# Optimization experiments

Measured on AMD Instinct MI355X. Metric: run time of the kernel, lower is better.

The kernel has to match this reference:

```python
import jax, jax.numpy as jnp
import numpy as np
from jax import lax


def setup_inputs() -> dict:
    key = jax.random.key(0)
    k1, k2, k3 = jax.random.split(key, 3)
    B, T, D, H = 128, 1024, 512, 512
    x = jax.random.normal(k1, (B, T, D), dtype=jnp.float32)
    # scaled init to keep tanh out of hard saturation
    W_ih = jax.random.normal(k2, (D, H), dtype=jnp.float32) / np.sqrt(D)
    W_hh = jax.random.normal(k3, (H, H), dtype=jnp.float32) / np.sqrt(H)
    b = jnp.zeros((H,), dtype=jnp.float32)
    return {"x": x, "W_ih": W_ih, "W_hh": W_hh, "b": b}


def reference(x, W_ih, W_hh, b):
    # Vanilla RNN: h_t = tanh(x_t @ W_ih + h_{t-1} @ W_hh + b)
    # return_sequences=False -> final hidden state (batch, hidden)
    B = x.shape[0]
    H = W_hh.shape[0]
    # Precompute the large input-to-hidden projection for all timesteps at once.
    xp = jnp.einsum('btd,dh->bth', x, W_ih) + b  # (B, T, H)
    xp_t = jnp.swapaxes(xp, 0, 1)                # (T, B, H) for scan over time

    def step(h, xp_step):
        h_new = jnp.tanh(xp_step + h @ W_hh)
        return h_new, None

    h0 = jnp.zeros((B, H), dtype=x.dtype)
    h_final, _ = lax.scan(step, h0, xp_t)
    return h_final
```

## Files before the change

### kernel.cpp

```cpp
#include <hip/hip_runtime.h>
#include <hip/hip_fp16.h>

typedef _Float16 half8 __attribute__((ext_vector_type(8)));
typedef _Float16 half4v __attribute__((ext_vector_type(4)));
typedef float floatx4 __attribute__((ext_vector_type(4)));

constexpr int BN = 128;
constexpr int T  = 1024;
constexpr int D  = 512;
constexpr int H  = 512;

constexpr size_t OFF_WIHT  = 0;
constexpr size_t OFF_WHHT  = 524288;
constexpr size_t OFF_HX    = 1048576;
constexpr size_t OFF_FLAGS = 1048576 + 262144;
constexpr size_t OFF_XP    = 2097152;

__device__ __forceinline__ float fast_tanh(float x) {
    float e = __expf(2.0f * x);
    return 1.0f - 2.0f / (e + 1.0f);
}

struct u64x2_s { unsigned long long a, b; };

__global__ __launch_bounds__(256) void prep_transpose(
    const float* __restrict__ Wih, const float* __restrict__ Whh,
    _Float16* __restrict__ WihT, _Float16* __restrict__ WhhT,
    int* __restrict__ flags)
{
    if (blockIdx.x == 0 && blockIdx.y == 0 && blockIdx.z == 0 && threadIdx.x < 16)
        flags[threadIdx.x * 16] = -1;

    __shared__ float tile[32][33];
    const float* src = (blockIdx.z == 0) ? Wih : Whh;
    _Float16* dst    = (blockIdx.z == 0) ? WihT : WhhT;
    const int tx = threadIdx.x & 31;
    const int ty = threadIdx.x >> 5;
    const int kbase = blockIdx.y * 32;
    const int nbase = blockIdx.x * 32;
    for (int r = 0; r < 4; ++r)
        tile[ty + r * 8][tx] = src[(size_t)(kbase + ty + r * 8) * 512 + nbase + tx];
    __syncthreads();
    for (int r = 0; r < 4; ++r)
        dst[(size_t)(nbase + ty + r * 8) * 512 + kbase + tx] =
            (_Float16)tile[tx][ty + r * 8];
}

__global__ __launch_bounds__(256) void xp_gemm(
    const float* __restrict__ x, const _Float16* __restrict__ WT,
    const float* __restrict__ bias, _Float16* __restrict__ xp)
{
    __shared__ _Float16 As[128][40];
    __shared__ _Float16 Bs[128][40];
    const int tid  = threadIdx.x;
    const int lane = tid & 63;
    const int w    = tid >> 6;
    const int wm   = w & 1, wn = w >> 1;
    const int l15  = lane & 15, q = lane >> 4;
    const size_t mbase = (size_t)blockIdx.y * 128;
    const int    nbase = blockIdx.x * 128;

    floatx4 acc[4][4];
    for (int i = 0; i < 4; ++i)
        for (int j = 0; j < 4; ++j)
            acc[i][j] = (floatx4){0.f, 0.f, 0.f, 0.f};

    for (int kt = 0; kt < 16; ++kt) {
        const int k0 = kt * 32;
        {
            const int k4 = (tid & 7) * 4;
            const int row0 = tid >> 3;
            for (int r = 0; r < 4; ++r) {
                const int row = row0 + r * 32;
                const float4 v = *(const float4*)&x[(mbase + row) * D + k0 + k4];
                half4v hv;
                hv[0] = (_Float16)v.x; hv[1] = (_Float16)v.y;
                hv[2] = (_Float16)v.z; hv[3] = (_Float16)v.w;
                *(half4v*)&As[row][k4] = hv;
            }
        }
        {
            const int k8 = (tid & 3) * 8;
            const int n0 = tid >> 2;
            for (int r = 0; r < 2; ++r) {
                const int n = n0 + r * 64;
                *(half8*)&Bs[n][k8] =
                    *(const half8*)&WT[(size_t)(nbase + n) * D + k0 + k8];
            }
        }
        __syncthreads();
        half8 a[4], b[4];
        for (int i = 0; i < 4; ++i)
            a[i] = *(const half8*)&As[wm * 64 + i * 16 + l15][q * 8];
        for (int j = 0; j < 4; ++j)
            b[j] = *(const half8*)&Bs[wn * 64 + j * 16 + l15][q * 8];
        for (int i = 0; i < 4; ++i)
            for (int j = 0; j < 4; ++j)
                acc[i][j] = __builtin_amdgcn_mfma_f32_16x16x32_f16(
                    a[i], b[j], acc[i][j], 0, 0, 0);
        __syncthreads();
    }
    float bc[4];
    for (int j = 0; j < 4; ++j)
        bc[j] = bias[nbase + wn * 64 + j * 16 + l15];
    for (int i = 0; i < 4; ++i)
        for (int r = 0; r < 4; ++r) {
            const size_t row = mbase + wm * 64 + i * 16 + q * 4 + r;
            const int b_row = (int)(row >> 10);
            const int tt    = (int)(row & 1023);
            _Float16* dst = &xp[((size_t)tt * BN + b_row) * H];
            for (int j = 0; j < 4; ++j) {
                const int col = nbase + wn * 64 + j * 16 + l15;
                dst[col] = (_Float16)(acc[i][j][r] + bc[j]);
            }
        }
}

__global__ __launch_bounds__(512, 2) void rnn_scan(
    const _Float16* __restrict__ xp, const _Float16* __restrict__ WT,
    float* __restrict__ out, _Float16* __restrict__ hx, int* __restrict__ flags)
{
    __shared__ _Float16 hbuf[2][4096];

    const int bid  = blockIdx.x;
    const int half = bid >> 3;
    const int g    = bid & 7;
    const int peer16 = (bid ^ 8) * 16;
    const int bid16  = bid * 16;
    const int tid  = threadIdx.x;
    const int lane = tid & 63;
    const int w    = tid >> 6;
    const int l15  = lane & 15;
    const int q    = lane >> 4;

    const int nbase = half * 256 + w * 32;
    const _Float16* wr0 = WT + (size_t)(nbase + 0  + l15) * H + q * 8;
    const _Float16* wr1 = WT + (size_t)(nbase + 16 + l15) * H + q * 8;

    half8 wa[16][2];
#pragma unroll
    for (int j = 0; j < 16; ++j) {
        const int c = (j < 8) ? (half * 8 + j) : ((half ^ 1) * 8 + (j - 8));
        wa[j][0] = *(const half8*)&wr0[c * 32];
        wa[j][1] = *(const half8*)&wr1[c * 32];
        asm volatile("" : "+a"(wa[j][0]), "+a"(wa[j][1]));
    }

    const int ebase = ((w * 4 + (q >> 1)) * 16 + l15) * 8 + (q & 1) * 4;

    {
        const _Float16* x0 = xp + ((size_t)g * 16 + l15) * H + nbase + q * 4;
        half4v v0 = *(const half4v*)&x0[0];
        half4v v1 = *(const half4v*)&x0[16];
        half4v hn0, hn1;
#pragma unroll
        for (int r = 0; r < 4; ++r) {
            hn0[r] = (_Float16)fast_tanh((float)v0[r]);
            hn1[r] = (_Float16)fast_tanh((float)v1[r]);
        }
        _Float16* hxo = hx + ((size_t)(1 * 8 + g) * 2 + half) * 4096;
        __hip_atomic_store((unsigned long long*)hxo + (ebase >> 2),
                           __builtin_bit_cast(unsigned long long, hn0),
                           __ATOMIC_RELAXED, __HIP_MEMORY_SCOPE_AGENT);
        __hip_atomic_store((unsigned long long*)hxo + ((ebase + 256) >> 2),
                           __builtin_bit_cast(unsigned long long, hn1),
                           __ATOMIC_RELAXED, __HIP_MEMORY_SCOPE_AGENT);
        *(half4v*)&hbuf[1][ebase]       = hn0;
        *(half4v*)&hbuf[1][ebase + 256] = hn1;
        __syncthreads();
        if (tid == 0)
            __hip_atomic_store(&flags[bid16], 0, __ATOMIC_RELAXED,
                               __HIP_MEMORY_SCOPE_AGENT);
    }

    const _Float16* xlane = xp + ((size_t)g * 16 + l15) * H + nbase + q * 4;
    const int poff64 = q * 32 + l15 * 2;

    for (int t = 1; t < T; ++t) {
        int f = __hip_atomic_load(&flags[peer16], __ATOMIC_RELAXED,
                                  __HIP_MEMORY_SCOPE_AGENT);
        __builtin_amdgcn_sched_barrier(0);

        const _Float16* xt = xlane + (size_t)t * (BN * H);
        const half4v xpv0 = *(const half4v*)&xt[0];
        const half4v xpv1 = *(const half4v*)&xt[16];

        const _Float16* hbo = &hbuf[t & 1][(q * 16 + l15) * 8];
        half8 hfA[8];
#pragma unroll
        for (int c8 = 0; c8 < 8; ++c8)
            hfA[c8] = *(const half8*)&hbo[c8 * 512];
        floatx4 acc0 = (floatx4){0.f,0.f,0.f,0.f};
        floatx4 acc1 = (floatx4){0.f,0.f,0.f,0.f};
#pragma unroll
        for (int c8 = 0; c8 < 8; ++c8) {
            acc0 = __builtin_amdgcn_mfma_f32_16x16x32_f16(wa[c8][0], hfA[c8], acc0, 0, 0, 0);
            acc1 = __builtin_amdgcn_mfma_f32_16x16x32_f16(wa[c8][1], hfA[c8], acc1, 0, 0, 0);
        }

        if (f < t - 1) {
            do {
                __builtin_amdgcn_s_sleep(1);
                f = __hip_atomic_load(&flags[peer16], __ATOMIC_RELAXED,
                                      __HIP_MEMORY_SCOPE_AGENT);
            } while (f < t - 1);
        }
        asm volatile("" : "+v"(f));

        const unsigned long long* ps64 = (const unsigned long long*)hx
            + ((size_t)((t & 1) * 8 + g) * 2 + (half ^ 1)) * 1024
            + poff64 + (f >> 31);
        half8 hfB[8];
#pragma unroll
        for (int c8 = 0; c8 < 8; ++c8) {
            unsigned long long d0 = __hip_atomic_load(&ps64[c8 * 128 + 0],
                                    __ATOMIC_RELAXED, __HIP_MEMORY_SCOPE_AGENT);
            unsigned long long d1 = __hip_atomic_load(&ps64[c8 * 128 + 1],
                                    __ATOMIC_RELAXED, __HIP_MEMORY_SCOPE_AGENT);
            hfB[c8] = __builtin_bit_cast(half8, u64x2_s{d0, d1});
        }

#pragma unroll
        for (int c8 = 0; c8 < 8; ++c8) {
            acc0 = __builtin_amdgcn_mfma_f32_16x16x32_f16(wa[8 + c8][0], hfB[c8], acc0, 0, 0, 0);
            acc1 = __builtin_amdgcn_mfma_f32_16x16x32_f16(wa[8 + c8][1], hfB[c8], acc1, 0, 0, 0);
        }

        if (t < T - 1) {
            half4v hn0, hn1;
#pragma unroll
            for (int r = 0; r < 4; ++r) {
                hn0[r] = (_Float16)fast_tanh(acc0[r] + (float)xpv0[r]);
                hn1[r] = (_Float16)fast_tanh(acc1[r] + (float)xpv1[r]);
            }
            _Float16* hxo = hx + ((size_t)(((t + 1) & 1) * 8 + g) * 2 + half) * 4096;
            __hip_atomic_store((unsigned long long*)hxo + (ebase >> 2),
                               __builtin_bit_cast(unsigned long long, hn0),
                               __ATOMIC_RELAXED, __HIP_MEMORY_SCOPE_AGENT);
            __hip_atomic_store((unsigned long long*)hxo + ((ebase + 256) >> 2),
                               __builtin_bit_cast(unsigned long long, hn1),
                               __ATOMIC_RELAXED, __HIP_MEMORY_SCOPE_AGENT);
            _Float16* ho = hbuf[(t + 1) & 1];
            *(half4v*)&ho[ebase]       = hn0;
            *(half4v*)&ho[ebase + 256] = hn1;
            __syncthreads();
            if (tid == 0)
                __hip_atomic_store(&flags[bid16], t, __ATOMIC_RELAXED,
                                   __HIP_MEMORY_SCOPE_AGENT);
        } else {
            float4 o0, o1;
            o0.x = fast_tanh(acc0[0] + (float)xpv0[0]);
            o0.y = fast_tanh(acc0[1] + (float)xpv0[1]);
            o0.z = fast_tanh(acc0[2] + (float)xpv0[2]);
            o0.w = fast_tanh(acc0[3] + (float)xpv0[3]);
            o1.x = fast_tanh(acc1[0] + (float)xpv1[0]);
            o1.y = fast_tanh(acc1[1] + (float)xpv1[1]);
            o1.z = fast_tanh(acc1[2] + (float)xpv1[2]);
            o1.w = fast_tanh(acc1[3] + (float)xpv1[3]);
            float* ob = &out[((size_t)g * 16 + l15) * H + nbase + q * 4];
            *(float4*)&ob[0]  = o0;
            *(float4*)&ob[16] = o1;
        }
    }
}

extern "C" void kernel_launch(void* const* d_in, const int* in_sizes, int n_in,
                              void* d_out, int out_size, void* d_ws, size_t ws_size,
                              hipStream_t stream)
{
    const float* x   = (const float*)d_in[0];
    const float* Wih = (const float*)d_in[1];
    const float* Whh = (const float*)d_in[2];
    const float* b   = (const float*)d_in[3];
    float* out = (float*)d_out;

    char* ws = (char*)d_ws;
    _Float16* WihT = (_Float16*)(ws + OFF_WIHT);
    _Float16* WhhT = (_Float16*)(ws + OFF_WHHT);
    _Float16* hx   = (_Float16*)(ws + OFF_HX);
    int*      flags = (int*)(ws + OFF_FLAGS);
    _Float16* xp   = (_Float16*)(ws + OFF_XP);

    prep_transpose<<<dim3(16, 16, 2), 256, 0, stream>>>(Wih, Whh, WihT, WhhT, flags);
    xp_gemm<<<dim3(4, 1024), 256, 0, stream>>>(x, WihT, b, xp);
    rnn_scan<<<16, 512, 0, stream>>>(xp, WhhT, out, hx, flags);
}
```

Before: 3.574 ms.

## Replace flag-based peer handshake with tagged data words polled directly

```diff
diff --git a/kernel.cpp b/kernel.cpp
--- a/kernel.cpp
+++ b/kernel.cpp
@@ -4,32 +4,40 @@
 typedef _Float16 half8 __attribute__((ext_vector_type(8)));
 typedef _Float16 half4v __attribute__((ext_vector_type(4)));
 typedef float floatx4 __attribute__((ext_vector_type(4)));
+typedef unsigned int uint;
+typedef unsigned long long u64;
 
 constexpr int BN = 128;
 constexpr int T  = 1024;
 constexpr int D  = 512;
 constexpr int H  = 512;
 
-constexpr size_t OFF_WIHT  = 0;
-constexpr size_t OFF_WHHT  = 524288;
-constexpr size_t OFF_HX    = 1048576;
-constexpr size_t OFF_FLAGS = 1048576 + 262144;
-constexpr size_t OFF_XP    = 2097152;
+constexpr size_t OFF_WIHT = 0;
+constexpr size_t OFF_WHHT = 524288;
+constexpr size_t OFF_HX   = 1048576;
+constexpr size_t OFF_XP   = 2097152;
 
 __device__ __forceinline__ float fast_tanh(float x) {
     float e = __expf(2.0f * x);
     return 1.0f - 2.0f / (e + 1.0f);
 }
 
-struct u64x2_s { unsigned long long a, b; };
+struct U2 { uint lo, hi; };
+struct U4 { uint x, y, z, w; };
+
+__device__ __forceinline__ u64 pack_q(uint dataw, uint tag) {
+    return (u64)dataw | ((u64)tag << 32);
+}
 
 __global__ __launch_bounds__(256) void prep_transpose(
     const float* __restrict__ Wih, const float* __restrict__ Whh,
     _Float16* __restrict__ WihT, _Float16* __restrict__ WhhT,
-    int* __restrict__ flags)
-{
-    if (blockIdx.x == 0 && blockIdx.y == 0 && blockIdx.z == 0 && threadIdx.x < 16)
-        flags[threadIdx.x * 16] = -1;
+    u64* __restrict__ hxq)
+{
+    if (blockIdx.z == 0) {
+        const int bi = blockIdx.y * 16 + blockIdx.x;
+        hxq[(size_t)bi * 256 + threadIdx.x] = 0ULL;
+    }
 
     __shared__ float tile[32][33];
     const float* src = (blockIdx.z == 0) ? Wih : Whh;
@@ -116,17 +124,56 @@
         }
 }
 
+__device__ __forceinline__ void publish_own(u64* base, int eq,
+                                            half4v hn0, half4v hn1, uint tag)
+{
+    const U2 a = __builtin_bit_cast(U2, hn0);
+    const U2 b = __builtin_bit_cast(U2, hn1);
+    __hip_atomic_store(&base[eq + 0],   pack_q(a.lo, tag),
+                       __ATOMIC_RELAXED, __HIP_MEMORY_SCOPE_AGENT);
+    __hip_atomic_store(&base[eq + 1],   pack_q(a.hi, tag),
+                       __ATOMIC_RELAXED, __HIP_MEMORY_SCOPE_AGENT);
+    __hip_atomic_store(&base[eq + 128], pack_q(b.lo, tag),
+                       __ATOMIC_RELAXED, __HIP_MEMORY_SCOPE_AGENT);
+    __hip_atomic_store(&base[eq + 129], pack_q(b.hi, tag),
+                       __ATOMIC_RELAXED, __HIP_MEMORY_SCOPE_AGENT);
+}
+
+__device__ __forceinline__ void poll32(const u64* __restrict__ pr, int qb,
+                                       uint want, half8* dst)
+{
+    u64 v[32];
+    for (int it = 0; it < 1024; ++it) {
+#pragma unroll
+        for (int c = 0; c < 8; ++c)
+#pragma unroll
+            for (int j = 0; j < 4; ++j)
+                v[c * 4 + j] = __hip_atomic_load(&pr[c * 256 + qb + j],
+                               __ATOMIC_RELAXED, __HIP_MEMORY_SCOPE_AGENT);
+        uint bad = 0;
+#pragma unroll
+        for (int k = 0; k < 32; ++k)
+            bad |= ((uint)(v[k] >> 32)) ^ want;
+        if (!__any(bad != 0)) break;
+        __builtin_amdgcn_s_sleep(2);
+    }
+#pragma unroll
+    for (int c = 0; c < 8; ++c) {
+        const U4 d = { (uint)v[c * 4 + 0], (uint)v[c * 4 + 1],
+                       (uint)v[c * 4 + 2], (uint)v[c * 4 + 3] };
+        dst[c] = __builtin_bit_cast(half8, d);
+    }
+}
+
 __global__ __launch_bounds__(512, 2) void rnn_scan(
     const _Float16* __restrict__ xp, const _Float16* __restrict__ WT,
-    float* __restrict__ out, _Float16* __restrict__ hx, int* __restrict__ flags)
+    float* __restrict__ out, u64* __restrict__ hxq)
 {
     __shared__ _Float16 hbuf[2][4096];
 
     const int bid  = blockIdx.x;
     const int half = bid >> 3;
     const int g    = bid & 7;
-    const int peer16 = (bid ^ 8) * 16;
-    const int bid16  = bid * 16;
     const int tid  = threadIdx.x;
     const int lane = tid & 63;
     const int w    = tid >> 6;
@@ -147,6 +194,13 @@
     }
 
     const int ebase = ((w * 4 + (q >> 1)) * 16 + l15) * 8 + (q & 1) * 4;
+    const int eq    = ebase >> 1;
+    const int qb    = q * 64 + l15 * 4;
+
+    u64* own0 = hxq + ((size_t)(0 * 8 + g) * 2 + half) * 2048;
+    u64* own1 = hxq + ((size_t)(1 * 8 + g) * 2 + half) * 2048;
+    const u64* peer0 = hxq + ((size_t)(0 * 8 + g) * 2 + (half ^ 1)) * 2048;
+    const u64* peer1 = hxq + ((size_t)(1 * 8 + g) * 2 + (half ^ 1)) * 2048;
 
     {
         const _Float16* x0 = xp + ((size_t)g * 16 + l15) * H + nbase + q * 4;
@@ -158,29 +212,15 @@
             hn0[r] = (_Float16)fast_tanh((float)v0[r]);
             hn1[r] = (_Float16)fast_tanh((float)v1[r]);
         }
-        _Float16* hxo = hx + ((size_t)(1 * 8 + g) * 2 + half) * 4096;
-        __hip_atomic_store((unsigned long long*)hxo + (ebase >> 2),
-                           __builtin_bit_cast(unsigned long long, hn0),
-                           __ATOMIC_RELAXED, __HIP_MEMORY_SCOPE_AGENT);
-        __hip_atomic_store((unsigned long long*)hxo + ((ebase + 256) >> 2),
-                           __builtin_bit_cast(unsigned long long, hn1),
-                           __ATOMIC_RELAXED, __HIP_MEMORY_SCOPE_AGENT);
+        publish_own(own1, eq, hn0, hn1, 1u);
         *(half4v*)&hbuf[1][ebase]       = hn0;
         *(half4v*)&hbuf[1][ebase + 256] = hn1;
         __syncthreads();
-        if (tid == 0)
-            __hip_atomic_store(&flags[bid16], 0, __ATOMIC_RELAXED,
-                               __HIP_MEMORY_SCOPE_AGENT);
     }
 
     const _Float16* xlane = xp + ((size_t)g * 16 + l15) * H + nbase + q * 4;
-    const int poff64 = q * 32 + l15 * 2;
 
     for (int t = 1; t < T; ++t) {
-        int f = __hip_atomic_load(&flags[peer16], __ATOMIC_RELAXED,
-                                  __HIP_MEMORY_SCOPE_AGENT);
-        __builtin_amdgcn_sched_barrier(0);
-
         const _Float16* xt = xlane + (size_t)t * (BN * H);
         const half4v xpv0 = *(const half4v*)&xt[0];
         const half4v xpv1 = *(const half4v*)&xt[16];
@@ -198,27 +238,9 @@
             acc1 = __builtin_amdgcn_mfma_f32_16x16x32_f16(wa[c8][1], hfA[c8], acc1, 0, 0, 0);
         }
 
-        if (f < t - 1) {
-            do {
-                __builtin_amdgcn_s_sleep(1);
-                f = __hip_atomic_load(&flags[peer16], __ATOMIC_RELAXED,
-                                      __HIP_MEMORY_SCOPE_AGENT);
-            } while (f < t - 1);
-        }
-        asm volatile("" : "+v"(f));
-
-        const unsigned long long* ps64 = (const unsigned long long*)hx
-            + ((size_t)((t & 1) * 8 + g) * 2 + (half ^ 1)) * 1024
-            + poff64 + (f >> 31);
+        const u64* pr = (t & 1) ? peer1 : peer0;
         half8 hfB[8];
-#pragma unroll
-        for (int c8 = 0; c8 < 8; ++c8) {
-            unsigned long long d0 = __hip_atomic_load(&ps64[c8 * 128 + 0],
-                                    __ATOMIC_RELAXED, __HIP_MEMORY_SCOPE_AGENT);
-            unsigned long long d1 = __hip_atomic_load(&ps64[c8 * 128 + 1],
-                                    __ATOMIC_RELAXED, __HIP_MEMORY_SCOPE_AGENT);
-            hfB[c8] = __builtin_bit_cast(half8, u64x2_s{d0, d1});
-        }
+        poll32(pr, qb, (uint)t, hfB);
 
 #pragma unroll
         for (int c8 = 0; c8 < 8; ++c8) {
@@ -233,20 +255,14 @@
                 hn0[r] = (_Float16)fast_tanh(acc0[r] + (float)xpv0[r]);
                 hn1[r] = (_Float16)fast_tanh(acc1[r] + (float)xpv1[r]);
             }
-            _Float16* hxo = hx + ((size_t)(((t + 1) & 1) * 8 + g) * 2 + half) * 4096;
-            __hip_atomic_store((unsigned long long*)hxo + (ebase >> 2),
-                               __builtin_bit_cast(unsigned long long, hn0),
-                               __ATOMIC_RELAXED, __HIP_MEMORY_SCOPE_AGENT);
-            __hip_atomic_store((unsigned long long*)hxo + ((ebase + 256) >> 2),
-                               __builtin_bit_cast(unsigned long long, hn1),
-                               __ATOMIC_RELAXED, __HIP_MEMORY_SCOPE_AGENT);
+            publish_own(((t + 1) & 1) ? own1 : own0, eq, hn0, hn1, (uint)(t + 1));
             _Float16* ho = hbuf[(t + 1) & 1];
             *(half4v*)&ho[ebase]       = hn0;
             *(half4v*)&ho[ebase + 256] = hn1;
-            __syncthreads();
-            if (tid == 0)
-                __hip_atomic_store(&flags[bid16], t, __ATOMIC_RELAXED,
-                                   __HIP_MEMORY_SCOPE_AGENT);
+            asm volatile("s_waitcnt lgkmcnt(0)" ::: "memory");
+            __builtin_amdgcn_sched_barrier(0);
+            __builtin_amdgcn_s_barrier();
+            __builtin_amdgcn_sched_barrier(0);
         } else {
             float4 o0, o1;
             o0.x = fast_tanh(acc0[0] + (float)xpv0[0]);
@@ -277,11 +293,10 @@
     char* ws = (char*)d_ws;
     _Float16* WihT = (_Float16*)(ws + OFF_WIHT);
     _Float16* WhhT = (_Float16*)(ws + OFF_WHHT);
-    _Float16* hx   = (_Float16*)(ws + OFF_HX);
-    int*      flags = (int*)(ws + OFF_FLAGS);
+    u64*      hxq  = (u64*)(ws + OFF_HX);
     _Float16* xp   = (_Float16*)(ws + OFF_XP);
 
-    prep_transpose<<<dim3(16, 16, 2), 256, 0, stream>>>(Wih, Whh, WihT, WhhT, flags);
+    prep_transpose<<<dim3(16, 16, 2), 256, 0, stream>>>(Wih, Whh, WihT, WhhT, hxq);
     xp_gemm<<<dim3(4, 1024), 256, 0, stream>>>(x, WihT, b, xp);
-    rnn_scan<<<16, 512, 0, stream>>>(xp, WhhT, out, hx, flags);
-}
+    rnn_scan<<<16, 512, 0, stream>>>(xp, WhhT, out, hxq);
+}
```

After: 5.492 ms. 1.54x slower.
